# Optimization experiments

Measured on AMD Instinct MI355X. Metric: run time of the kernel, lower is better.

Reference implementation:

```python
import jax, jax.numpy as jnp
import numpy as np

N_NODES = 50000
N_EDGES = 800000
IN_DIM = 232
EMB = 300
HID = 2 * EMB
N_LAYERS = 5
BN_EPS = 1e-5


def setup_inputs() -> dict:
    key = jax.random.key(0)
    ks = jax.random.split(key, 12)
    x = jax.random.normal(ks[0], (N_NODES, IN_DIM), dtype=jnp.float32)
    edge_index = jax.random.randint(ks[1], (2, N_EDGES), 0, N_NODES, dtype=jnp.int64)
    edge_attr = jax.random.normal(ks[2], (N_EDGES, 9), dtype=jnp.float32)
    s_in = 1.0 / np.sqrt(IN_DIM)
    s_emb = 1.0 / np.sqrt(EMB)
    s_hid = 1.0 / np.sqrt(HID)
    lin_in_w = jax.random.uniform(ks[3], (IN_DIM, EMB), jnp.float32, -s_in, s_in)
    lin_in_b = jax.random.uniform(ks[4], (EMB,), jnp.float32, -s_in, s_in)
    w1 = jax.random.uniform(ks[5], (N_LAYERS, EMB, HID), jnp.float32, -s_emb, s_emb)
    b1 = jax.random.uniform(ks[6], (N_LAYERS, HID), jnp.float32, -s_emb, s_emb)
    gamma = jnp.ones((N_LAYERS, HID), jnp.float32)
    beta = jnp.zeros((N_LAYERS, HID), jnp.float32)
    w2 = jax.random.uniform(ks[7], (N_LAYERS, HID, EMB), jnp.float32, -s_hid, s_hid)
    b2 = jax.random.uniform(ks[8], (N_LAYERS, EMB), jnp.float32, -s_hid, s_hid)
    return {"x": x, "edge_index": edge_index, "edge_attr": edge_attr,
            "lin_in_w": lin_in_w, "lin_in_b": lin_in_b,
            "w1": w1, "b1": b1, "gamma": gamma, "beta": beta,
            "w2": w2, "b2": b2}


def reference(x, edge_index, edge_attr, lin_in_w, lin_in_b, w1, b1, gamma, beta, w2, b2):
    n = x.shape[0]
    self_loop = jnp.arange(n, dtype=edge_index.dtype)
    src = jnp.concatenate([edge_index[0], self_loop])  # [E+N]
    dst = jnp.concatenate([edge_index[1], self_loop])
    # input layer linear (232 -> emb)
    h = x @ lin_in_w + lin_in_b  # [N, EMB]
    num_layer = w1.shape[0]
    for l in range(num_layer):
        # gather messages at src, scatter-add at dst (GIN aggr='add' with self loops)
        agg = jax.ops.segment_sum(h[src], dst, num_segments=n)  # [N, EMB]
        # MLP: Linear -> BatchNorm1d (train-mode batch stats) -> ReLU -> Linear
        z = agg @ w1[l] + b1[l]  # [N, HID]
        mu = z.mean(axis=0)
        var = z.var(axis=0)  # biased, as torch BatchNorm uses for normalization
        z = (z - mu) * jax.lax.rsqrt(var + BN_EPS) * gamma[l] + beta[l]
        z = jax.nn.relu(z)
        h_new = z @ w2[l] + b2[l]  # [N, EMB]
        # GNN wrapper: relu between layers, none after the last (drop_ratio=0)
        h = h_new if l == num_layer - 1 else jax.nn.relu(h_new)
    return h  # JK='last'
```

## Files before the change

kernel.cpp:

```cpp
#include <hip/hip_runtime.h>
#include <cstdint>
#include <cstddef>

#define NNODES 50000
#define NEDGES 800000
#define IN_DIM 232
#define EMB 300
#define HID 600
#define NLAYERS 5
#define BN_EPS 1e-5f

#define MPAD 50048
#define K0P 256
#define K1P 320
#define K2P 608
#define N0P 384
#define N1P 640
#define MT_TILES 391
#define CSTR 140

typedef unsigned short ushort_t;
typedef __attribute__((ext_vector_type(8))) short bf16x8;
typedef __attribute__((ext_vector_type(4))) float f32x4;

__device__ __forceinline__ float b2f(ushort_t u) {
    unsigned int x = (unsigned int)u << 16;
    return __builtin_bit_cast(float, x);
}
__device__ __forceinline__ ushort_t f2b(float f) {
    unsigned int x = __builtin_bit_cast(unsigned int, f);
    unsigned int r = (x + 0x7fffu + ((x >> 16) & 1u)) >> 16;
    return (ushort_t)r;
}

__device__ __forceinline__ void gl_lds16(const void* gsrc, void* ldst) {
    __builtin_amdgcn_global_load_lds(
        (const __attribute__((address_space(1))) void*)gsrc,
        (__attribute__((address_space(3))) void*)ldst, 16, 0, 0);
}

__global__ void detect_mode_kernel(const unsigned int* __restrict__ ei, int* __restrict__ mode) {
    if (threadIdx.x == 0 && blockIdx.x == 0) {
        int nz = 0;
        for (int i = 0; i < 256; ++i) nz += (ei[2 * i + 1] != 0u);
        *mode = (nz == 0) ? 1 : 0;
    }
}
__device__ __forceinline__ int load_edge(const int* ei, int mode, long long idx) {
    if (mode) return (int)((const long long*)ei)[idx];
    return ei[idx];
}

__global__ void hist_kernel(const int* __restrict__ ei, const int* __restrict__ mode,
                            int* __restrict__ deg) {
    int i = blockIdx.x * blockDim.x + threadIdx.x;
    if (i >= NEDGES) return;
    int d = load_edge(ei, *mode, (long long)NEDGES + i);
    atomicAdd(&deg[d], 1);
}

__global__ void scan_block_sums(const int* __restrict__ deg, int* __restrict__ bsum, int n) {
    __shared__ int s[256];
    int t = threadIdx.x;
    int i = blockIdx.x * 256 + t;
    s[t] = (i < n) ? deg[i] : 0;
    __syncthreads();
    for (int off = 128; off > 0; off >>= 1) {
        if (t < off) s[t] += s[t + off];
        __syncthreads();
    }
    if (t == 0) bsum[blockIdx.x] = s[0];
}

__global__ void scan_bsums(int* __restrict__ bsum, int nb) {
    __shared__ int s[256];
    int t = threadIdx.x;
    int v = (t < nb) ? bsum[t] : 0;
    s[t] = v;
    __syncthreads();
    for (int off = 1; off < 256; off <<= 1) {
        int u = (t >= off) ? s[t - off] : 0;
        __syncthreads();
        s[t] += u;
        __syncthreads();
    }
    if (t < nb) bsum[t] = s[t] - v;
}

__global__ void scan_final(const int* __restrict__ deg, const int* __restrict__ bsum,
                           int* __restrict__ offs, int* __restrict__ cursor, int n) {
    __shared__ int s[256];
    int t = threadIdx.x;
    int i = blockIdx.x * 256 + t;
    int v = (i < n) ? deg[i] : 0;
    s[t] = v;
    __syncthreads();
    for (int off = 1; off < 256; off <<= 1) {
        int u = (t >= off) ? s[t - off] : 0;
        __syncthreads();
        s[t] += u;
        __syncthreads();
    }
    int excl = s[t] - v + bsum[blockIdx.x];
    if (i < n) {
        offs[i] = excl;
        cursor[i] = excl;
        if (i == n - 1) offs[n] = excl + v;
    }
}

__global__ void fill_csr(const int* __restrict__ ei, const int* __restrict__ mode,
                         int* __restrict__ cursor, int* __restrict__ csr) {
    int i = blockIdx.x * blockDim.x + threadIdx.x;
    if (i >= NEDGES) return;
    int m = *mode;
    int s = load_edge(ei, m, i);
    int d = load_edge(ei, m, (long long)NEDGES + i);
    int p = atomicAdd(&cursor[d], 1);
    csr[p] = s;
}

__global__ __launch_bounds__(256) void cast_x_kernel(const float* __restrict__ x,
                                                     ushort_t* __restrict__ o) {
    int idx = blockIdx.x * 256 + threadIdx.x;
    if (idx >= NNODES * 32) return;
    int row = idx >> 5, g = idx & 31;
    ushort_t* dst = o + (size_t)row * K0P + g * 8;
    if (g < 29) {
        const float* src = x + (size_t)row * IN_DIM + g * 8;
        float4 a = *(const float4*)src;
        float4 b = *(const float4*)(src + 4);
        ushort_t tmp[8] = {f2b(a.x), f2b(a.y), f2b(a.z), f2b(a.w),
                           f2b(b.x), f2b(b.y), f2b(b.z), f2b(b.w)};
        *(uint4*)dst = *(const uint4*)tmp;
    } else {
        uint4 zz = {0, 0, 0, 0};
        *(uint4*)dst = zz;
    }
}
__global__ void conv_lin_kernel(const float* __restrict__ w, ushort_t* __restrict__ o) {
    int idx = blockIdx.x * 256 + threadIdx.x;
    if (idx >= N0P * K0P) return;
    int n = idx >> 8, k = idx & 255;
    float v = (n < EMB && k < IN_DIM) ? w[(size_t)k * EMB + n] : 0.f;
    o[idx] = f2b(v);
}
__global__ void conv_w1_kernel(const float* __restrict__ w, ushort_t* __restrict__ o) {
    int idx = blockIdx.x * 256 + threadIdx.x;
    if (idx >= NLAYERS * N1P * K1P) return;
    int l = idx / (N1P * K1P);
    int r = idx - l * (N1P * K1P);
    int n = r / K1P, k = r - n * K1P;
    float v = (n < HID && k < EMB) ? w[((size_t)l * EMB + k) * HID + n] : 0.f;
    o[idx] = f2b(v);
}
__global__ void conv_w2_kernel(const float* __restrict__ w, ushort_t* __restrict__ o) {
    int idx = blockIdx.x * 256 + threadIdx.x;
    if (idx >= NLAYERS * N0P * K2P) return;
    int l = idx / (N0P * K2P);
    int r = idx - l * (N0P * K2P);
    int n = r / K2P, k = r - n * K2P;
    float v = (n < EMB && k < HID) ? w[((size_t)l * HID + k) * EMB + n] : 0.f;
    o[idx] = f2b(v);
}

__global__ __launch_bounds__(256) void aggregate_bf16(
    const ushort_t* __restrict__ h, ushort_t* __restrict__ agg,
    const int* __restrict__ offs, const int* __restrict__ csr) {
    const int w = blockIdx.x * 4 + (threadIdx.x >> 6);
    const int lane = threadIdx.x & 63;
    const int wid0 = w * 2, wid1 = wid0 + 1;
    if (wid0 >= NNODES) return;
    const bool hasb = lane < 11;
    float a0[4], a1[4] = {0.f, 0.f, 0.f, 0.f};
    float c0[4], c1[4] = {0.f, 0.f, 0.f, 0.f};
    {
        const ushort4* r0 = (const ushort4*)(h + (size_t)wid0 * K1P);
        const ushort4* r1 = (const ushort4*)(h + (size_t)wid1 * K1P);
        ushort4 v0 = r0[lane], v1 = r1[lane];
        a0[0] = b2f(v0.x); a0[1] = b2f(v0.y); a0[2] = b2f(v0.z); a0[3] = b2f(v0.w);
        c0[0] = b2f(v1.x); c0[1] = b2f(v1.y); c0[2] = b2f(v1.z); c0[3] = b2f(v1.w);
        if (hasb) {
            ushort4 w0 = r0[64 + lane], w1 = r1[64 + lane];
            a1[0] = b2f(w0.x); a1[1] = b2f(w0.y); a1[2] = b2f(w0.z); a1[3] = b2f(w0.w);
            c1[0] = b2f(w1.x); c1[1] = b2f(w1.y); c1[2] = b2f(w1.z); c1[3] = b2f(w1.w);
        }
    }
    int p0 = offs[wid0], e0 = offs[wid0 + 1];
    int p1 = e0, e1 = offs[wid1 + 1];

    while (p0 + 4 <= e0 && p1 + 4 <= e1) {
        int s0[4], s1[4];
#pragma unroll
        for (int u = 0; u < 4; ++u) { s0[u] = csr[p0 + u]; s1[u] = csr[p1 + u]; }
        ushort4 x0[4], x1[4], y0[4], y1[4];
#pragma unroll
        for (int u = 0; u < 4; ++u) {
            const ushort4* r0 = (const ushort4*)(h + (size_t)s0[u] * K1P);
            const ushort4* r1 = (const ushort4*)(h + (size_t)s1[u] * K1P);
            x0[u] = r0[lane];
            x1[u] = r1[lane];
            if (hasb) { y0[u] = r0[64 + lane]; y1[u] = r1[64 + lane]; }
        }
#pragma unroll
        for (int u = 0; u < 4; ++u) {
            a0[0] += b2f(x0[u].x); a0[1] += b2f(x0[u].y); a0[2] += b2f(x0[u].z); a0[3] += b2f(x0[u].w);
            c0[0] += b2f(x1[u].x); c0[1] += b2f(x1[u].y); c0[2] += b2f(x1[u].z); c0[3] += b2f(x1[u].w);
            if (hasb) {
                a1[0] += b2f(y0[u].x); a1[1] += b2f(y0[u].y); a1[2] += b2f(y0[u].z); a1[3] += b2f(y0[u].w);
                c1[0] += b2f(y1[u].x); c1[1] += b2f(y1[u].y); c1[2] += b2f(y1[u].z); c1[3] += b2f(y1[u].w);
            }
        }
        p0 += 4; p1 += 4;
    }

    while (p0 < e0 && p1 < e1) {
        const ushort4* r0 = (const ushort4*)(h + (size_t)csr[p0] * K1P); ++p0;
        const ushort4* r1 = (const ushort4*)(h + (size_t)csr[p1] * K1P); ++p1;
        ushort4 v0 = r0[lane];
        ushort4 v1 = r1[lane];
        a0[0] += b2f(v0.x); a0[1] += b2f(v0.y); a0[2] += b2f(v0.z); a0[3] += b2f(v0.w);
        c0[0] += b2f(v1.x); c0[1] += b2f(v1.y); c0[2] += b2f(v1.z); c0[3] += b2f(v1.w);
        if (hasb) {
            ushort4 w0 = r0[64 + lane];
            ushort4 w1 = r1[64 + lane];
            a1[0] += b2f(w0.x); a1[1] += b2f(w0.y); a1[2] += b2f(w0.z); a1[3] += b2f(w0.w);
            c1[0] += b2f(w1.x); c1[1] += b2f(w1.y); c1[2] += b2f(w1.z); c1[3] += b2f(w1.w);
        }
    }
    while (p0 < e0) {
        const ushort4* r0 = (const ushort4*)(h + (size_t)csr[p0] * K1P); ++p0;
        ushort4 v0 = r0[lane];
        a0[0] += b2f(v0.x); a0[1] += b2f(v0.y); a0[2] += b2f(v0.z); a0[3] += b2f(v0.w);
        if (hasb) {
            ushort4 w0 = r0[64 + lane];
            a1[0] += b2f(w0.x); a1[1] += b2f(w0.y); a1[2] += b2f(w0.z); a1[3] += b2f(w0.w);
        }
    }
    while (p1 < e1) {
        const ushort4* r1 = (const ushort4*)(h + (size_t)csr[p1] * K1P); ++p1;
        ushort4 v1 = r1[lane];
        c0[0] += b2f(v1.x); c0[1] += b2f(v1.y); c0[2] += b2f(v1.z); c0[3] += b2f(v1.w);
        if (hasb) {
            ushort4 w1 = r1[64 + lane];
            c1[0] += b2f(w1.x); c1[1] += b2f(w1.y); c1[2] += b2f(w1.z); c1[3] += b2f(w1.w);
        }
    }
    ushort4* o0 = (ushort4*)(agg + (size_t)wid0 * K1P);
    ushort4* o1 = (ushort4*)(agg + (size_t)wid1 * K1P);
    ushort4 ov;
    ov.x = f2b(a0[0]); ov.y = f2b(a0[1]); ov.z = f2b(a0[2]); ov.w = f2b(a0[3]);
    o0[lane] = ov;
    ov.x = f2b(c0[0]); ov.y = f2b(c0[1]); ov.z = f2b(c0[2]); ov.w = f2b(c0[3]);
    o1[lane] = ov;
    if (hasb) {
        ov.x = f2b(a1[0]); ov.y = f2b(a1[1]); ov.z = f2b(a1[2]); ov.w = f2b(a1[3]);
        o0[64 + lane] = ov;
        ov.x = f2b(c1[0]); ov.y = f2b(c1[1]); ov.z = f2b(c1[2]); ov.w = f2b(c1[3]);
        o1[64 + lane] = ov;
    }
    if (lane < 5) {
        ushort4 zz; zz.x = zz.y = zz.z = zz.w = 0;
        o0[75 + lane] = zz;
        o1[75 + lane] = zz;
    }
}

template <int PRO, int RELU, int STATS, int OUT_BF16>
__global__ __launch_bounds__(256) void gemm_mfma(
    const ushort_t* __restrict__ A, int lda,
    const ushort_t* __restrict__ Bt, int ldb,
    const float* __restrict__ bias,
    void* __restrict__ C, int ldc, int M, int N, int K,
    const float* __restrict__ pscale, const float* __restrict__ pshift, int Kreal,
    float* __restrict__ partials, int NB) {
    __shared__ ushort_t sh[PRO ? 17920 : 32768];
    __shared__ float psS[PRO ? 640 : 4];
    __shared__ float pfS[PRO ? 640 : 4];

    const int bid = blockIdx.x;
    const int xcd = bid & 7, slot = bid >> 3;
    const int mt = (slot / NB) * 8 + xcd;
    if (mt >= MT_TILES) return;
    const int nt = slot % NB;
    const int m0 = mt << 7, n0 = nt << 7;

    const int tid = threadIdx.x;
    const int wave = tid >> 6, lane = tid & 63;
    const int wm = wave >> 1, wn = wave & 1;
    const int NT = K >> 5;

    const int srow = lane >> 2;
    const int schunk = ((lane & 3) ^ ((lane >> 3) & 3)) << 3;
    const ushort_t* bP = Bt + (size_t)(n0 + (wave << 5) + srow) * ldb + schunk;
    const ushort_t* aPg = A + (size_t)(m0 + (wave << 5) + srow) * lda + schunk;
    const ushort_t* aPr = A + (size_t)(m0 + (wave << 5) + srow) * lda + ((lane & 3) << 3);
    const int a16 = lda << 4, b16 = ldb << 4;
    const int ldsW = wave << 10;

    const int fr = lane & 15, fq = lane >> 4;
    const int rdoff = (fq ^ ((fr >> 1) & 3)) << 3;

    f32x4 acc[4][4];
#pragma unroll
    for (int i = 0; i < 4; ++i)
#pragma unroll
        for (int j = 0; j < 4; ++j) acc[i][j] = {0.f, 0.f, 0.f, 0.f};

    if (PRO) {
        for (int i = tid; i < 640; i += 256) {
            psS[i] = (i < Kreal) ? pscale[i] : 0.f;
            pfS[i] = (i < Kreal) ? pshift[i] : 0.f;
        }
        __syncthreads();
    }

    if (!PRO) {
        const ushort_t* aN = aPg;
        const ushort_t* bN = bP;
        gl_lds16(aN, sh + ldsW);
        gl_lds16(aN + a16, sh + ldsW + 512);
        gl_lds16(bN, sh + 16384 + ldsW);
        gl_lds16(bN + b16, sh + 16384 + ldsW + 512);
        aN += 32; bN += 32;
        gl_lds16(aN, sh + 4096 + ldsW);
        gl_lds16(aN + a16, sh + 4096 + ldsW + 512);
        gl_lds16(bN, sh + 20480 + ldsW);
        gl_lds16(bN + b16, sh + 20480 + ldsW + 512);
        aN += 32; bN += 32;

        for (int t = 0; t < NT; ++t) {
            const int cb = t & 3;
            if (t + 2 < NT) {
                const int sb = (t + 2) & 3;
                gl_lds16(aN, sh + (sb << 12) + ldsW);
                gl_lds16(aN + a16, sh + (sb << 12) + ldsW + 512);
                gl_lds16(bN, sh + 16384 + (sb << 12) + ldsW);
                gl_lds16(bN + b16, sh + 16384 + (sb << 12) + ldsW + 512);
                aN += 32; bN += 32;
                asm volatile("s_waitcnt vmcnt(8)" ::: "memory");
            } else if (t + 1 < NT) {
                asm volatile("s_waitcnt vmcnt(4)" ::: "memory");
            } else {
                asm volatile("s_waitcnt vmcnt(0)" ::: "memory");
            }
            __builtin_amdgcn_s_barrier();
            __builtin_amdgcn_sched_barrier(0);

            const ushort_t* ASc = sh + (cb << 12);
            const ushort_t* BSc = sh + 16384 + (cb << 12);
            bf16x8 af[4], bf[4];
#pragma unroll
            for (int mi = 0; mi < 4; ++mi)
                af[mi] = *(const bf16x8*)&ASc[((wm << 6) + (mi << 4) + fr) * 32 + rdoff];
#pragma unroll
            for (int nj = 0; nj < 4; ++nj)
                bf[nj] = *(const bf16x8*)&BSc[((wn << 6) + (nj << 4) + fr) * 32 + rdoff];
#pragma unroll
            for (int mi = 0; mi < 4; ++mi)
#pragma unroll
                for (int nj = 0; nj < 4; ++nj)
                    acc[mi][nj] = __builtin_amdgcn_mfma_f32_16x16x32_bf16(af[mi], bf[nj], acc[mi][nj], 0, 0, 0);

            __builtin_amdgcn_sched_barrier(0);
        }
    } else {
        ushort_t* const AS0 = sh;
        ushort_t* const AS1 = sh + 4096;
        ushort_t* const BS0 = sh + 8192;
        ushort_t* const BS1 = sh + 12288;
        uint4 ar0, ar1;
        const ushort_t* aNext;
        const ushort_t* bNext = bP + 32;
        ar0 = *(const uint4*)aPr;
        ar1 = *(const uint4*)(aPr + a16);
        gl_lds16(bP, BS0 + ldsW);
        gl_lds16(bP + b16, BS0 + ldsW + 512);
        aNext = aPr + 32;

        int cur = 0;
        for (int t = 0; t < NT; ++t) {
            ushort_t* const ASc = cur ? AS1 : AS0;
            ushort_t* const BSn = cur ? BS0 : BS1;
            ushort_t* const BSc = cur ? BS1 : BS0;
            asm volatile("s_waitcnt vmcnt(2)" ::: "memory");
            const int kb = (t << 5) + ((lane & 3) << 3);
            float4 psa = *(const float4*)&psS[kb];
            float4 psb = *(const float4*)&psS[kb + 4];
            float4 pfa = *(const float4*)&pfS[kb];
            float4 pfb = *(const float4*)&pfS[kb + 4];
            float ps[8] = {psa.x, psa.y, psa.z, psa.w, psb.x, psb.y, psb.z, psb.w};
            float pf[8] = {pfa.x, pfa.y, pfa.z, pfa.w, pfb.x, pfb.y, pfb.z, pfb.w};
            bf16x8 w0, w1;
            const ushort_t* u0 = (const ushort_t*)&ar0;
            const ushort_t* u1 = (const ushort_t*)&ar1;
#pragma unroll
            for (int j = 0; j < 8; ++j) {
                float v0 = b2f(u0[j]) * ps[j] + pf[j];
                float v1 = b2f(u1[j]) * ps[j] + pf[j];
                w0[j] = (short)f2b(v0 > 0.f ? v0 : 0.f);
                w1[j] = (short)f2b(v1 > 0.f ? v1 : 0.f);
            }
            ushort_t* dA = ASc + ((wave << 5) + srow) * 32 + schunk;
            *(bf16x8*)dA = w0;
            *(bf16x8*)(dA + 16 * 32) = w1;
            if (t + 1 < NT) {
                ar0 = *(const uint4*)aNext;
                ar1 = *(const uint4*)(aNext + a16);
                gl_lds16(bNext, BSn + ldsW);
                gl_lds16(bNext + b16, BSn + ldsW + 512);
                aNext += 32; bNext += 32;
                asm volatile("s_waitcnt vmcnt(4) lgkmcnt(0)" ::: "memory");
            } else {
                asm volatile("s_waitcnt vmcnt(0) lgkmcnt(0)" ::: "memory");
            }
            __builtin_amdgcn_s_barrier();
            __builtin_amdgcn_sched_barrier(0);

            bf16x8 af[4], bf[4];
#pragma unroll
            for (int mi = 0; mi < 4; ++mi)
                af[mi] = *(const bf16x8*)&ASc[((wm << 6) + (mi << 4) + fr) * 32 + rdoff];
#pragma unroll
            for (int nj = 0; nj < 4; ++nj)
                bf[nj] = *(const bf16x8*)&BSc[((wn << 6) + (nj << 4) + fr) * 32 + rdoff];
#pragma unroll
            for (int mi = 0; mi < 4; ++mi)
#pragma unroll
                for (int nj = 0; nj < 4; ++nj)
                    acc[mi][nj] = __builtin_amdgcn_mfma_f32_16x16x32_bf16(af[mi], bf[nj], acc[mi][nj], 0, 0, 0);

            __builtin_amdgcn_sched_barrier(0);
            __builtin_amdgcn_s_barrier();
            cur ^= 1;
        }
    }

    if (STATS) {
        float s1[4] = {0.f, 0.f, 0.f, 0.f}, s2[4] = {0.f, 0.f, 0.f, 0.f};
#pragma unroll
        for (int nj = 0; nj < 4; ++nj) {
            const int col = n0 + (wn << 6) + (nj << 4) + fr;
            if (col < N) {
                const float bv = bias[col];
#pragma unroll
                for (int mi = 0; mi < 4; ++mi) {
                    const int rbase = m0 + (wm << 6) + (mi << 4) + (fq << 2);
#pragma unroll
                    for (int r = 0; r < 4; ++r) {
                        if (rbase + r < M) {
                            float v = acc[mi][nj][r] + bv;
                            if (RELU) v = v > 0.f ? v : 0.f;
                            s1[nj] += v; s2[nj] += v * v;
                        }
                    }
                }
            }
        }
#pragma unroll
        for (int nj = 0; nj < 4; ++nj) {
            s1[nj] += __shfl_xor(s1[nj], 16);
            s1[nj] += __shfl_xor(s1[nj], 32);
            s2[nj] += __shfl_xor(s2[nj], 16);
            s2[nj] += __shfl_xor(s2[nj], 32);
        }
        if (lane < 16) {
            float* pw = partials + (size_t)(mt * 2 + wm) * 2 * 640;
#pragma unroll
            for (int nj = 0; nj < 4; ++nj) {
                const int col = n0 + (wn << 6) + (nj << 4) + lane;
                if (col < N) {
                    pw[col] = s1[nj];
                    pw[640 + col] = s2[nj];
                }
            }
        }
    }

    __syncthreads();
    if (OUT_BF16) {
        ushort_t* ct = sh;
#pragma unroll
        for (int nj = 0; nj < 4; ++nj) {
            const int col_l = (wn << 6) + (nj << 4) + fr;
            const int col = n0 + col_l;
            const float bv = (col < N) ? bias[col] : 0.f;
#pragma unroll
            for (int mi = 0; mi < 4; ++mi) {
                const int rl0 = (wm << 6) + (mi << 4) + (fq << 2);
#pragma unroll
                for (int r = 0; r < 4; ++r) {
                    float v = acc[mi][nj][r] + bv;
                    if (RELU) v = v > 0.f ? v : 0.f;
                    ct[(rl0 + r) * CSTR + col_l] = f2b(v);
                }
            }
        }
        __syncthreads();
        const int rr = tid >> 1, half = tid & 1;
        const int grow = m0 + rr;
        if (grow < M) {
            const ushort_t* src = ct + rr * CSTR + (half << 6);
            ushort_t* dst = (ushort_t*)C + (size_t)grow * ldc + n0 + (half << 6);
#pragma unroll
            for (int c = 0; c < 8; ++c) {
                const int gc = n0 + (half << 6) + (c << 3);
                if (gc + 7 < N) {
                    uint2 u0 = *(const uint2*)(src + (c << 3));
                    uint2 u1 = *(const uint2*)(src + (c << 3) + 4);
                    uint4 o; o.x = u0.x; o.y = u0.y; o.z = u1.x; o.w = u1.y;
                    *(uint4*)(dst + (c << 3)) = o;
                } else {
                    for (int j = 0; j < 8; ++j)
                        if (gc + j < N) dst[(c << 3) + j] = src[(c << 3) + j];
                }
            }
        }
    } else {
        float* ctf = (float*)sh;
#pragma unroll
        for (int ph = 0; ph < 2; ++ph) {
            if (wm == ph) {
#pragma unroll
                for (int nj = 0; nj < 4; ++nj) {
                    const int col_l = (wn << 6) + (nj << 4) + fr;
                    const int col = n0 + col_l;
                    const float bv = (col < N) ? bias[col] : 0.f;
#pragma unroll
                    for (int mi = 0; mi < 4; ++mi) {
                        const int rl0 = (mi << 4) + (fq << 2);
#pragma unroll
                        for (int r = 0; r < 4; ++r) {
                            float v = acc[mi][nj][r] + bv;
                            if (RELU) v = v > 0.f ? v : 0.f;
                            ctf[(rl0 + r) * CSTR + col_l] = v;
                        }
                    }
                }
            }
            __syncthreads();
            const int rr = tid >> 2, q = tid & 3;
            const int grow = m0 + (ph << 6) + rr;
            if (grow < M) {
                const float* src = ctf + rr * CSTR + (q << 5);
                float* dst = (float*)C + (size_t)grow * ldc + n0 + (q << 5);
#pragma unroll
                for (int c = 0; c < 8; ++c) {
                    const int gc = n0 + (q << 5) + (c << 2);
                    if (gc + 3 < N) {
                        *(float4*)(dst + (c << 2)) = *(const float4*)(src + (c << 2));
                    } else {
                        for (int j = 0; j < 4; ++j)
                            if (gc + j < N) dst[(c << 2) + j] = src[(c << 2) + j];
                    }
                }
            }
            __syncthreads();
        }
    }
}

__global__ __launch_bounds__(256) void bn_reduce(
    const float* __restrict__ partials, const float* __restrict__ gamma,
    const float* __restrict__ beta, float* __restrict__ pscale,
    float* __restrict__ pshift, float invM) {
    const int c = blockIdx.x;
    const int t = threadIdx.x;
    float s1 = 0.f, s2 = 0.f;
    for (int i = t; i < MT_TILES * 2; i += 256) {
        const float* pw = partials + (size_t)i * 2 * 640;
        s1 += pw[c];
        s2 += pw[640 + c];
    }
    __shared__ float r1[256], r2[256];
    r1[t] = s1; r2[t] = s2;
    __syncthreads();
    for (int off = 128; off > 0; off >>= 1) {
        if (t < off) { r1[t] += r1[t + off]; r2[t] += r2[t + off]; }
        __syncthreads();
    }
    if (t == 0) {
        float mu = r1[0] * invM;
        float var = r2[0] * invM - mu * mu;
        float rs = rsqrtf(var + BN_EPS);
        float g = gamma[c] * rs;
        pscale[c] = g;
        pshift[c] = beta[c] - mu * g;
    }
}

extern "C" void kernel_launch(void* const* d_in, const int* in_sizes, int n_in,
                              void* d_out, int out_size, void* d_ws, size_t ws_size,
                              hipStream_t stream) {
    const float* x = (const float*)d_in[0];
    const int* ei = (const int*)d_in[1];
    const float* lin_in_w = (const float*)d_in[3];
    const float* lin_in_b = (const float*)d_in[4];
    const float* w1 = (const float*)d_in[5];
    const float* b1 = (const float*)d_in[6];
    const float* gamma = (const float*)d_in[7];
    const float* beta = (const float*)d_in[8];
    const float* w2 = (const float*)d_in[9];
    const float* b2 = (const float*)d_in[10];
    float* out = (float*)d_out;

    char* p = (char*)d_ws;
    auto alloc = [&](size_t bytes) {
        char* r = p;
        p += (bytes + 255) & ~(size_t)255;
        return r;
    };
    ushort_t* xb  = (ushort_t*)alloc((size_t)MPAD * K0P * 2);
    ushort_t* h   = (ushort_t*)alloc((size_t)MPAD * K1P * 2);
    ushort_t* agg = (ushort_t*)alloc((size_t)MPAD * K1P * 2);
    ushort_t* z   = (ushort_t*)alloc((size_t)MPAD * K2P * 2);
    ushort_t* lint = (ushort_t*)alloc((size_t)N0P * K0P * 2);
    ushort_t* w1t  = (ushort_t*)alloc((size_t)NLAYERS * N1P * K1P * 2);
    ushort_t* w2t  = (ushort_t*)alloc((size_t)NLAYERS * N0P * K2P * 2);
    int* deg    = (int*)alloc(NNODES * 4);
    int* cursor = (int*)alloc(NNODES * 4);
    int* offs   = (int*)alloc((NNODES + 1) * 4);
    int* bsum   = (int*)alloc(1024);
    int* csr    = (int*)alloc((size_t)NEDGES * 4);
    float* partials = (float*)alloc((size_t)MT_TILES * 2 * 2 * 640 * 4);
    float* pscale = (float*)alloc(HID * 4);
    float* pshift = (float*)alloc(HID * 4);
    int* mode   = (int*)alloc(256);
    (void)ws_size; (void)in_sizes; (void)n_in; (void)out_size;

    hipMemsetAsync(deg, 0, NNODES * 4, stream);
    hipMemsetAsync(h + (size_t)NNODES * K1P, 0, (size_t)(MPAD - NNODES) * K1P * 2, stream);

    detect_mode_kernel<<<1, 64, 0, stream>>>((const unsigned int*)ei, mode);
    hist_kernel<<<(NEDGES + 255) / 256, 256, 0, stream>>>(ei, mode, deg);
    const int nb = (NNODES + 255) / 256;
    scan_block_sums<<<nb, 256, 0, stream>>>(deg, bsum, NNODES);
    scan_bsums<<<1, 256, 0, stream>>>(bsum, nb);
    scan_final<<<nb, 256, 0, stream>>>(deg, bsum, offs, cursor, NNODES);
    fill_csr<<<(NEDGES + 255) / 256, 256, 0, stream>>>(ei, mode, cursor, csr);

    cast_x_kernel<<<(NNODES * 32 + 255) / 256, 256, 0, stream>>>(x, xb);
    conv_lin_kernel<<<(N0P * K0P + 255) / 256, 256, 0, stream>>>(lin_in_w, lint);
    conv_w1_kernel<<<(NLAYERS * N1P * K1P + 255) / 256, 256, 0, stream>>>(w1, w1t);
    conv_w2_kernel<<<(NLAYERS * N0P * K2P + 255) / 256, 256, 0, stream>>>(w2, w2t);

    const int G3 = 8 * 49 * 3;
    const int G5 = 8 * 49 * 5;

    gemm_mfma<0, 0, 0, 1><<<G3, 256, 0, stream>>>(
        xb, K0P, lint, K0P, lin_in_b, h, K1P, NNODES, EMB, K0P,
        nullptr, nullptr, 0, nullptr, 3);

    for (int l = 0; l < NLAYERS; ++l) {
        aggregate_bf16<<<(NNODES / 2 + 3) / 4, 256, 0, stream>>>(h, agg, offs, csr);
        gemm_mfma<0, 0, 1, 1><<<G5, 256, 0, stream>>>(
            agg, K1P, w1t + (size_t)l * N1P * K1P, K1P, b1 + (size_t)l * HID,
            z, K2P, NNODES, HID, K1P,
            nullptr, nullptr, 0, partials, 5);
        bn_reduce<<<HID, 256, 0, stream>>>(
            partials, gamma + (size_t)l * HID, beta + (size_t)l * HID,
            pscale, pshift, 1.f / NNODES);
        if (l < NLAYERS - 1) {
            gemm_mfma<1, 1, 0, 1><<<G3, 256, 0, stream>>>(
                z, K2P, w2t + (size_t)l * N0P * K2P, K2P, b2 + (size_t)l * EMB,
                h, K1P, NNODES, EMB, K2P,
                pscale, pshift, HID, nullptr, 3);
        } else {
            gemm_mfma<1, 0, 0, 0><<<G3, 256, 0, stream>>>(
                z, K2P, w2t + (size_t)l * N0P * K2P, K2P, b2 + (size_t)l * EMB,
                out, EMB, NNODES, EMB, K2P,
                pscale, pshift, HID, nullptr, 3);
        }
    }
}
```

Baseline: 1.119 ms.

## Sort nodes by degree so paired aggregation warps have balanced edge counts

Adds a counting sort of nodes by in-degree (per-block LDS histogram, single-block scan, scatter into a permutation) and makes the aggregation kernel process node pairs from that permutation. Each wave then handles two nodes of similar degree, so the joint 4-wide unrolled loop runs further before falling into a tail, and waves finish at similar times. The cost is three extra small kernels per call, an indirect perm lookup, and a loss of locality in the h row reads and agg row writes, since neighbouring waves no longer handle neighbouring node ids.

```diff
diff --git a/kernel.cpp b/kernel.cpp
--- a/kernel.cpp
+++ b/kernel.cpp
@@ -18,6 +18,7 @@
 #define N1P 640
 #define MT_TILES 391
 #define CSTR 140
+#define NBH 196
 
 typedef unsigned short ushort_t;
 typedef __attribute__((ext_vector_type(8))) short bf16x8;
@@ -118,6 +119,58 @@
     int d = load_edge(ei, m, (long long)NEDGES + i);
     int p = atomicAdd(&cursor[d], 1);
     csr[p] = s;
+}
+
+__global__ __launch_bounds__(256) void deg_hist_lds(const int* __restrict__ offs,
+                                                    int* __restrict__ bh) {
+    __shared__ int lh[256];
+    const int t = threadIdx.x, j = blockIdx.x;
+    lh[t] = 0;
+    __syncthreads();
+    const int i = j * 256 + t;
+    if (i < NNODES) {
+        int d = offs[i + 1] - offs[i];
+        if (d > 255) d = 255;
+        atomicAdd(&lh[d], 1);
+    }
+    __syncthreads();
+    bh[j * 256 + t] = lh[t];
+}
+__global__ __launch_bounds__(256) void deg_scan2(int* __restrict__ bh) {
+    __shared__ int tot[256];
+    const int t = threadIdx.x;
+    int running = 0;
+    for (int j = 0; j < NBH; ++j) {
+        int v = bh[j * 256 + t];
+        bh[j * 256 + t] = running;
+        running += v;
+    }
+    tot[t] = running;
+    __syncthreads();
+    int v = tot[t];
+    for (int off = 1; off < 256; off <<= 1) {
+        int u = (t >= off) ? tot[t - off] : 0;
+        __syncthreads();
+        tot[t] += u;
+        __syncthreads();
+    }
+    const int base = tot[t] - v;
+    for (int j = 0; j < NBH; ++j) bh[j * 256 + t] += base;
+}
+__global__ __launch_bounds__(256) void deg_scatter_lds(const int* __restrict__ offs,
+                                                       const int* __restrict__ bh,
+                                                       int* __restrict__ perm) {
+    __shared__ int cur[256];
+    const int t = threadIdx.x, j = blockIdx.x;
+    cur[t] = bh[j * 256 + t];
+    __syncthreads();
+    const int i = j * 256 + t;
+    if (i < NNODES) {
+        int d = offs[i + 1] - offs[i];
+        if (d > 255) d = 255;
+        int pos = atomicAdd(&cur[d], 1);
+        perm[pos] = i;
+    }
 }
 
 __global__ __launch_bounds__(256) void cast_x_kernel(const float* __restrict__ x,
@@ -166,11 +219,12 @@
 
 __global__ __launch_bounds__(256) void aggregate_bf16(
     const ushort_t* __restrict__ h, ushort_t* __restrict__ agg,
-    const int* __restrict__ offs, const int* __restrict__ csr) {
+    const int* __restrict__ offs, const int* __restrict__ csr,
+    const int* __restrict__ perm) {
     const int w = blockIdx.x * 4 + (threadIdx.x >> 6);
     const int lane = threadIdx.x & 63;
-    const int wid0 = w * 2, wid1 = wid0 + 1;
-    if (wid0 >= NNODES) return;
+    if (w * 2 >= NNODES) return;
+    const int wid0 = perm[w * 2], wid1 = perm[w * 2 + 1];
     const bool hasb = lane < 11;
     float a0[4], a1[4] = {0.f, 0.f, 0.f, 0.f};
     float c0[4], c1[4] = {0.f, 0.f, 0.f, 0.f};
@@ -187,7 +241,7 @@
         }
     }
     int p0 = offs[wid0], e0 = offs[wid0 + 1];
-    int p1 = e0, e1 = offs[wid1 + 1];
+    int p1 = offs[wid1], e1 = offs[wid1 + 1];
 
     while (p0 + 4 <= e0 && p1 + 4 <= e1) {
         int s0[4], s1[4];
@@ -622,6 +676,8 @@
     int* offs   = (int*)alloc((NNODES + 1) * 4);
     int* bsum   = (int*)alloc(1024);
     int* csr    = (int*)alloc((size_t)NEDGES * 4);
+    int* bh     = (int*)alloc((size_t)NBH * 256 * 4);
+    int* perm   = (int*)alloc(NNODES * 4);
     float* partials = (float*)alloc((size_t)MT_TILES * 2 * 2 * 640 * 4);
     float* pscale = (float*)alloc(HID * 4);
     float* pshift = (float*)alloc(HID * 4);
@@ -639,6 +695,10 @@
     scan_final<<<nb, 256, 0, stream>>>(deg, bsum, offs, cursor, NNODES);
     fill_csr<<<(NEDGES + 255) / 256, 256, 0, stream>>>(ei, mode, cursor, csr);
 
+    deg_hist_lds<<<NBH, 256, 0, stream>>>(offs, bh);
+    deg_scan2<<<1, 256, 0, stream>>>(bh);
+    deg_scatter_lds<<<NBH, 256, 0, stream>>>(offs, bh, perm);
+
     cast_x_kernel<<<(NNODES * 32 + 255) / 256, 256, 0, stream>>>(x, xb);
     conv_lin_kernel<<<(N0P * K0P + 255) / 256, 256, 0, stream>>>(lin_in_w, lint);
     conv_w1_kernel<<<(NLAYERS * N1P * K1P + 255) / 256, 256, 0, stream>>>(w1, w1t);
@@ -652,7 +712,7 @@
         nullptr, nullptr, 0, nullptr, 3);
 
     for (int l = 0; l < NLAYERS; ++l) {
-        aggregate_bf16<<<(NNODES / 2 + 3) / 4, 256, 0, stream>>>(h, agg, offs, csr);
+        aggregate_bf16<<<(NNODES / 2 + 3) / 4, 256, 0, stream>>>(h, agg, offs, csr, perm);
         gemm_mfma<0, 0, 1, 1><<<G5, 256, 0, stream>>>(
             agg, K1P, w1t + (size_t)l * N1P * K1P, K1P, b1 + (size_t)l * HID,
             z, K2P, NNODES, HID, K1P,
```

Result: no change. 1.130 ms (+1.0%).
